# Optimization experiments

Hardware: AMD Instinct MI355X
Metric: run time of the kernel (lower is better)

The kernel has to match this reference:

```python
import jax, jax.numpy as jnp
import numpy as np

D_MODEL, D_INNER, D_STATE, D_CONV, DT_RANK = 2048, 4096, 16, 4, 128
B, T = 2, 1024


def setup_inputs() -> dict:
    key = jax.random.key(0)
    ks = jax.random.split(key, 8)
    dt_init_std = DT_RANK ** -0.5
    # dt bias init per the torch code: inv softplus of dt in [dt_min, dt_max]
    dt = jnp.exp(jax.random.uniform(ks[6], (D_INNER,)) * (np.log(0.1) - np.log(0.001)) + np.log(0.001))
    dt = jnp.clip(dt, 1e-4, None)
    dt_proj_b = dt + jnp.log(-jnp.expm1(-dt))
    A_log = jnp.log(jnp.tile(jnp.arange(1, D_STATE + 1, dtype=jnp.float32)[None, :], (D_INNER, 1)))
    return {
        "x": jax.random.normal(ks[0], (B, T, D_MODEL), jnp.float32),
        "h": jnp.zeros((B, D_INNER, D_STATE), jnp.float32),
        "conv_cache": jnp.zeros((B, D_INNER, D_CONV - 1), jnp.float32),
        "in_proj_w": jax.random.normal(ks[1], (2 * D_INNER, D_MODEL), jnp.float32) * 0.02,
        "conv_w": jax.random.normal(ks[2], (D_INNER, D_CONV), jnp.float32) * (1.0 / np.sqrt(D_CONV)),
        "conv_b": jnp.zeros((D_INNER,), jnp.float32),
        "x_proj_w": jax.random.normal(ks[3], (DT_RANK + 2 * D_STATE, D_INNER), jnp.float32) * 0.02,
        "dt_proj_w": jax.random.uniform(ks[4], (D_INNER, DT_RANK), jnp.float32, -dt_init_std, dt_init_std),
        "dt_proj_b": dt_proj_b,
        "A_log": A_log,
        "D_param": jnp.ones((D_INNER,), jnp.float32),
        "out_proj_w": jax.random.normal(ks[5], (D_MODEL, D_INNER), jnp.float32) * 0.02,
    }


def _forward(x, h, conv_cache, in_proj_w, conv_w, conv_b, x_proj_w,
             dt_proj_w, dt_proj_b, A_log, D_param, out_proj_w):
    Tlen = x.shape[1]
    xz = x @ in_proj_w.T                                  # (B,T,2*d_inner)
    xi, z = jnp.split(xz, 2, axis=-1)
    # causal depthwise conv with cache: concat history then valid conv
    xc = jnp.concatenate([jnp.swapaxes(conv_cache, 1, 2), xi], axis=1)  # (B,T+3,d_inner)
    new_conv_cache = jnp.swapaxes(xc[:, -(D_CONV - 1):, :], 1, 2)       # (B,d_inner,3)
    xconv = sum(xc[:, k:k + Tlen, :] * conv_w[:, k] for k in range(D_CONV)) + conv_b
    xs = jax.nn.silu(xconv)                               # (B,T,d_inner)
    # SSM params per step
    dbc = xs @ x_proj_w.T                                 # (B,T,dt_rank+2n)
    delta, Bm, Cm = jnp.split(dbc, [DT_RANK, DT_RANK + D_STATE], axis=-1)
    delta = jax.nn.softplus(delta @ dt_proj_w.T + dt_proj_b)  # (B,T,d_inner)
    A = -jnp.exp(A_log)                                   # (d_inner,n)
    dA = jnp.exp(jnp.einsum('btd,dn->btdn', delta, A))    # (B,T,d,n)
    dBx = jnp.einsum('btd,btn,btd->btdn', delta, Bm, xs)  # (B,T,d,n)

    def step(hc, inp):
        dA_t, dBx_t, C_t = inp
        hc = dA_t * hc + dBx_t                            # (B,d,n)
        return hc, jnp.einsum('bdn,bn->bd', hc, C_t)

    h_last, ys = jax.lax.scan(
        step, h,
        (jnp.moveaxis(dA, 1, 0), jnp.moveaxis(dBx, 1, 0), jnp.moveaxis(Cm, 1, 0)))
    y = jnp.moveaxis(ys, 0, 1) + D_param * xs             # (B,T,d_inner)
    out = (y * jax.nn.silu(z)) @ out_proj_w.T             # (B,T,d_model)
    return out, h_last, new_conv_cache


def reference(x, h, conv_cache, in_proj_w, conv_w, conv_b, x_proj_w,
              dt_proj_w, dt_proj_b, A_log, D_param, out_proj_w):
    return _forward(x, h, conv_cache, in_proj_w, conv_w, conv_b, x_proj_w,
                    dt_proj_w, dt_proj_b, A_log, D_param, out_proj_w)
```

## Files before the change

kernel.cpp:

```cpp
#include <hip/hip_runtime.h>
#include <hip/hip_bf16.h>
#include <math.h>

#define D_MODEL 2048
#define D_INNER 4096
#define D_STATE 16
#define D_CONV  4
#define DT_RANK 128
#define NB      2
#define TT      1024
#define M_TOT   (NB * TT)
#define NC      16
#define CL      64
#define TC      16

typedef __bf16 bf16x8_t __attribute__((ext_vector_type(8)));
typedef float  f32x4_t  __attribute__((ext_vector_type(4)));

__global__ __launch_bounds__(256) void fused_cast(
    const float* __restrict__ x,  const float* __restrict__ wi,
    const float* __restrict__ wo, const float* __restrict__ wx,
    const float* __restrict__ wdt,
    __bf16* __restrict__ x16,  __bf16* __restrict__ wi16,
    __bf16* __restrict__ wo16, __bf16* __restrict__ wx16,
    __bf16* __restrict__ wdt16, __bf16* __restrict__ dbc16)
{
    const size_t g = (size_t)blockIdx.x * 256 + threadIdx.x;
    const float* src; __bf16* dst; size_t off;
    if      (g < 524288)  { src = x;   dst = x16;   off = g; }
    else if (g < 2621440) { src = wi;  dst = wi16;  off = g - 524288; }
    else if (g < 3670016) { src = wo;  dst = wo16;  off = g - 2621440; }
    else if (g < 3801088) { off = g - 3670016; dst = wx16;
                            src = (g < 3751936) ? wx : nullptr; }
    else if (g < 3866624) { src = wdt; dst = wdt16; off = g - 3801088; }
    else                  { src = nullptr; dst = dbc16; off = g - 3866624; }

    bf16x8_t v;
    if (src) {
        const float4 f0 = ((const float4*)src)[2 * off];
        const float4 f1 = ((const float4*)src)[2 * off + 1];
        v[0] = (__bf16)f0.x; v[1] = (__bf16)f0.y; v[2] = (__bf16)f0.z; v[3] = (__bf16)f0.w;
        v[4] = (__bf16)f1.x; v[5] = (__bf16)f1.y; v[6] = (__bf16)f1.z; v[7] = (__bf16)f1.w;
    } else {
        v = (bf16x8_t)(__bf16)0.f;
    }
    ((bf16x8_t*)dst)[off] = v;
}

template <int EPI, int KSTEP, typename OutT>
__global__ __launch_bounds__(256) void gemm_bf16_nt(
    const __bf16* __restrict__ A, int lda,
    const __bf16* __restrict__ W, int ldw,
    OutT* __restrict__ C, int ldc,
    int Kloop, int Nmax, const float* __restrict__ bias)
{
    __shared__ __bf16 As[128 * KSTEP];
    __shared__ __bf16 Bs[128 * KSTEP];

    const int tid  = threadIdx.x;
    const int wave = tid >> 6;
    const int lane = tid & 63;
    const int m0 = blockIdx.y * 128;
    const int n0 = blockIdx.x * 128;
    const int mw = (wave >> 1) * 64;
    const int nw = (wave & 1) * 64;
    const int koff = blockIdx.z * Kloop;

    f32x4_t acc[4][4] = {};

    const int g0 = wave * 2;
    const int rA = g0 * 16 + (lane >> 2);
    const int kk = (lane & 3) * 8;

    const __bf16* gA0 = A + (size_t)(m0 + rA) * lda + kk + koff;
    const __bf16* gA1 = gA0 + (size_t)16 * lda;
    const __bf16* gB0 = W + (size_t)(n0 + rA) * ldw + kk + koff;
    const __bf16* gB1 = gB0 + (size_t)16 * ldw;

    __bf16* lA0 = &As[(size_t)g0 * 512];
    __bf16* lA1 = &As[(size_t)(g0 + 1) * 512];
    __bf16* lB0 = &Bs[(size_t)g0 * 512];
    __bf16* lB1 = &Bs[(size_t)(g0 + 1) * 512];

    const int fr = lane & 15;
    const int fk = (lane >> 4) * 8;

    for (int k0 = 0; k0 < Kloop; k0 += KSTEP) {
#pragma unroll
        for (int p = 0; p < KSTEP / 32; p++) {
            const int kp = k0 + p * 32;
            const int lp = p * 4096;
            __builtin_amdgcn_global_load_lds(
                (const __attribute__((address_space(1))) void*)(gA0 + kp),
                (__attribute__((address_space(3))) void*)(lA0 + lp), 16, 0, 0);
            __builtin_amdgcn_global_load_lds(
                (const __attribute__((address_space(1))) void*)(gA1 + kp),
                (__attribute__((address_space(3))) void*)(lA1 + lp), 16, 0, 0);
            __builtin_amdgcn_global_load_lds(
                (const __attribute__((address_space(1))) void*)(gB0 + kp),
                (__attribute__((address_space(3))) void*)(lB0 + lp), 16, 0, 0);
            __builtin_amdgcn_global_load_lds(
                (const __attribute__((address_space(1))) void*)(gB1 + kp),
                (__attribute__((address_space(3))) void*)(lB1 + lp), 16, 0, 0);
        }
        __syncthreads();

#pragma unroll
        for (int p = 0; p < KSTEP / 32; p++) {
            const int lp = p * 4096;
            bf16x8_t av[4], bv[4];
#pragma unroll
            for (int mt = 0; mt < 4; mt++)
                av[mt] = *(const bf16x8_t*)&As[lp + (mw + mt * 16 + fr) * 32 + fk];
#pragma unroll
            for (int nt = 0; nt < 4; nt++)
                bv[nt] = *(const bf16x8_t*)&Bs[lp + (nw + nt * 16 + fr) * 32 + fk];

#pragma unroll
            for (int mt = 0; mt < 4; mt++)
#pragma unroll
                for (int nt = 0; nt < 4; nt++)
                    acc[mt][nt] = __builtin_amdgcn_mfma_f32_16x16x32_bf16(
                        av[mt], bv[nt], acc[mt][nt], 0, 0, 0);
        }
        __syncthreads();
    }

    const int cn = n0 + nw + (lane & 15);
    const int rb = m0 + mw + (lane >> 4) * 4;
#pragma unroll
    for (int mt = 0; mt < 4; mt++)
#pragma unroll
        for (int nt = 0; nt < 4; nt++) {
            const int n = cn + nt * 16;
            if (n >= Nmax) continue;
#pragma unroll
            for (int r = 0; r < 4; r++) {
                float v = acc[mt][nt][r];
                OutT* p = &C[(size_t)(rb + mt * 16 + r) * ldc + n];
                if (EPI == 1) {
                    v += bias[n];
                    v = (v > 20.f) ? v : log1pf(__expf(v));
                    *p = (OutT)v;
                } else if (EPI == 2) {
                    atomicAdd((float*)p, v);
                } else {
                    *p = (OutT)v;
                }
            }
        }
}

__global__ __launch_bounds__(256) void gemm_dt(
    const float* __restrict__ A,
    const __bf16* __restrict__ W,
    float* __restrict__ C,
    const float* __restrict__ bias)
{
    __shared__ __bf16 As[128 * 32];
    __shared__ __bf16 Bs[128 * 32];

    const int tid  = threadIdx.x;
    const int wave = tid >> 6;
    const int lane = tid & 63;
    const int m0 = blockIdx.y * 128;
    const int n0 = blockIdx.x * 128;
    const int mw = (wave >> 1) * 64;
    const int nw = (wave & 1) * 64;

    f32x4_t acc[4][4] = {};

    const int g0 = wave * 2;
    const int rA = g0 * 16 + (lane >> 2);
    const int kk = (lane & 3) * 8;

    const float*  gA0 = A + (size_t)(m0 + rA) * 160 + kk;
    const float*  gA1 = gA0 + (size_t)16 * 160;
    const __bf16* gB0 = W + (size_t)(n0 + rA) * 128 + kk;
    const __bf16* gB1 = gB0 + (size_t)16 * 128;

    __bf16* lA0 = &As[(size_t)g0 * 512];
    __bf16* lA1 = &As[(size_t)(g0 + 1) * 512];
    __bf16* lB0 = &Bs[(size_t)g0 * 512];
    __bf16* lB1 = &Bs[(size_t)(g0 + 1) * 512];

    const int fr = lane & 15;
    const int fk = (lane >> 4) * 8;

    for (int k0 = 0; k0 < 128; k0 += 32) {
        const float4 a0 = *(const float4*)(gA0 + k0);
        const float4 a1 = *(const float4*)(gA0 + k0 + 4);
        const float4 a2 = *(const float4*)(gA1 + k0);
        const float4 a3 = *(const float4*)(gA1 + k0 + 4);
        bf16x8_t va, vb;
        va[0] = (__bf16)a0.x; va[1] = (__bf16)a0.y; va[2] = (__bf16)a0.z; va[3] = (__bf16)a0.w;
        va[4] = (__bf16)a1.x; va[5] = (__bf16)a1.y; va[6] = (__bf16)a1.z; va[7] = (__bf16)a1.w;
        vb[0] = (__bf16)a2.x; vb[1] = (__bf16)a2.y; vb[2] = (__bf16)a2.z; vb[3] = (__bf16)a2.w;
        vb[4] = (__bf16)a3.x; vb[5] = (__bf16)a3.y; vb[6] = (__bf16)a3.z; vb[7] = (__bf16)a3.w;
        ((bf16x8_t*)lA0)[lane] = va;
        ((bf16x8_t*)lA1)[lane] = vb;
        __builtin_amdgcn_global_load_lds(
            (const __attribute__((address_space(1))) void*)(gB0 + k0),
            (__attribute__((address_space(3))) void*)lB0, 16, 0, 0);
        __builtin_amdgcn_global_load_lds(
            (const __attribute__((address_space(1))) void*)(gB1 + k0),
            (__attribute__((address_space(3))) void*)lB1, 16, 0, 0);
        __syncthreads();

        bf16x8_t av[4], bv[4];
#pragma unroll
        for (int mt = 0; mt < 4; mt++)
            av[mt] = *(const bf16x8_t*)&As[(mw + mt * 16 + fr) * 32 + fk];
#pragma unroll
        for (int nt = 0; nt < 4; nt++)
            bv[nt] = *(const bf16x8_t*)&Bs[(nw + nt * 16 + fr) * 32 + fk];

#pragma unroll
        for (int mt = 0; mt < 4; mt++)
#pragma unroll
            for (int nt = 0; nt < 4; nt++)
                acc[mt][nt] = __builtin_amdgcn_mfma_f32_16x16x32_bf16(
                    av[mt], bv[nt], acc[mt][nt], 0, 0, 0);
        __syncthreads();
    }

    const int cn = n0 + nw + (lane & 15);
    const int rb = m0 + mw + (lane >> 4) * 4;
#pragma unroll
    for (int mt = 0; mt < 4; mt++)
#pragma unroll
        for (int nt = 0; nt < 4; nt++) {
            const int n = cn + nt * 16;
            const float bs = bias[n];
#pragma unroll
            for (int r = 0; r < 4; r++) {
                float v = acc[mt][nt][r] + bs;
                v = (v > 20.f) ? v : log1pf(__expf(v));
                C[(size_t)(rb + mt * 16 + r) * 4096 + n] = v;
            }
        }
}

__global__ __launch_bounds__(256) void conv_silu(
    const __bf16* __restrict__ xz16,
    const float* __restrict__ conv_cache,
    const float* __restrict__ conv_w,
    const float* __restrict__ conv_b,
    __bf16* __restrict__ xs16,
    float* __restrict__ cc_out)
{
    const int b  = blockIdx.z;
    const int d  = blockIdx.y * 256 + threadIdx.x;
    const int t0 = blockIdx.x * TC;

    const float4 w  = *(const float4*)&conv_w[d * 4];
    const float bias = conv_b[d];

    float v[TC + 3];
    if (t0 == 0) {
        v[0] = conv_cache[(b * D_INNER + d) * 3 + 0];
        v[1] = conv_cache[(b * D_INNER + d) * 3 + 1];
        v[2] = conv_cache[(b * D_INNER + d) * 3 + 2];
    } else {
        v[0] = (float)xz16[(size_t)(b * TT + t0 - 3) * 8192 + d];
        v[1] = (float)xz16[(size_t)(b * TT + t0 - 2) * 8192 + d];
        v[2] = (float)xz16[(size_t)(b * TT + t0 - 1) * 8192 + d];
    }
#pragma unroll
    for (int k = 0; k < TC; k++)
        v[k + 3] = (float)xz16[(size_t)(b * TT + t0 + k) * 8192 + d];

#pragma unroll
    for (int k = 0; k < TC; k++) {
        float c = v[k] * w.x + v[k + 1] * w.y + v[k + 2] * w.z + v[k + 3] * w.w + bias;
        float s = c / (1.f + __expf(-c));
        xs16[(size_t)(b * TT + t0 + k) * 4096 + d] = (__bf16)s;
    }

    if (t0 + TC == TT) {
        cc_out[(b * D_INNER + d) * 3 + 0] = v[TC];
        cc_out[(b * D_INNER + d) * 3 + 1] = v[TC + 1];
        cc_out[(b * D_INNER + d) * 3 + 2] = v[TC + 2];
    }
}

__global__ __launch_bounds__(256) void scan_phase_a(
    const float* __restrict__ delta_p,
    const float* __restrict__ dbc,
    const __bf16* __restrict__ xs16,
    const float* __restrict__ A_log,
    float* __restrict__ P,
    float* __restrict__ S)
{
    const int idx = blockIdx.x * 256 + threadIdx.x;
    const int sub = idx & 3;
    const int d   = (idx >> 2) & 4095;
    const int c   = (idx >> 14) & (NC - 1);
    const int b   = idx >> 18;

    const float4 Af = *(const float4*)&A_log[d * 16 + sub * 4];
    const float Ad0 = -__expf(Af.x), Ad1 = -__expf(Af.y);
    const float Ad2 = -__expf(Af.z), Ad3 = -__expf(Af.w);

    const int t0 = c * CL;
    const float*  pdelta = delta_p + (size_t)(b * TT + t0) * 4096 + d;
    const __bf16* px     = xs16 + (size_t)(b * TT + t0) * 4096 + d;
    const float*  pB     = dbc + ((size_t)b * TT + t0) * 160 + 128 + sub * 4;

    float h0 = 0.f, h1 = 0.f, h2 = 0.f, h3 = 0.f, sd = 0.f;
    for (int t = 0; t < CL; t++) {
        const float delta = pdelta[(size_t)t * 4096];
        const float xv    = (float)px[(size_t)t * 4096];
        const float4 Bv   = *(const float4*)&pB[(size_t)t * 160];
        const float dx = delta * xv;
        h0 = __expf(delta * Ad0) * h0 + dx * Bv.x;
        h1 = __expf(delta * Ad1) * h1 + dx * Bv.y;
        h2 = __expf(delta * Ad2) * h2 + dx * Bv.z;
        h3 = __expf(delta * Ad3) * h3 + dx * Bv.w;
        sd += delta;
    }
    const size_t o = ((size_t)(b * NC + c) * 4096 + d) * 16 + sub * 4;
    *(float4*)&P[o] = make_float4(__expf(Ad0 * sd), __expf(Ad1 * sd),
                                  __expf(Ad2 * sd), __expf(Ad3 * sd));
    *(float4*)&S[o] = make_float4(h0, h1, h2, h3);
}

__global__ __launch_bounds__(256) void scan_phase_c(
    const float* __restrict__ delta_p,
    const __bf16* __restrict__ xz16,
    const float* __restrict__ dbc,
    const __bf16* __restrict__ xs16,
    const float* __restrict__ P,
    const float* __restrict__ S,
    const float* __restrict__ h_in,
    const float* __restrict__ A_log,
    const float* __restrict__ D_param,
    __bf16* __restrict__ ys16,
    float* __restrict__ h_out)
{
    const int idx = blockIdx.x * 256 + threadIdx.x;
    const int sub = idx & 3;
    const int d   = (idx >> 2) & 4095;
    const int c   = (idx >> 14) & (NC - 1);
    const int b   = idx >> 18;

    const float4 Af = *(const float4*)&A_log[d * 16 + sub * 4];
    const float Ad0 = -__expf(Af.x), Ad1 = -__expf(Af.y);
    const float Ad2 = -__expf(Af.z), Ad3 = -__expf(Af.w);
    const float Dp = D_param[d];

    float4 hf = *(const float4*)&h_in[((size_t)b * 4096 + d) * 16 + sub * 4];
    float h0 = hf.x, h1 = hf.y, h2 = hf.z, h3 = hf.w;
    for (int cc = 0; cc < c; cc++) {
        const size_t o2 = ((size_t)(b * NC + cc) * 4096 + d) * 16 + sub * 4;
        const float4 p = *(const float4*)&P[o2];
        const float4 s = *(const float4*)&S[o2];
        h0 = p.x * h0 + s.x;
        h1 = p.y * h1 + s.y;
        h2 = p.z * h2 + s.z;
        h3 = p.w * h3 + s.w;
    }

    const int t0 = c * CL;
    const float*  pdelta = delta_p + (size_t)(b * TT + t0) * 4096 + d;
    const __bf16* pz     = xz16 + (size_t)(b * TT + t0) * 8192 + 4096 + d;
    const __bf16* px     = xs16 + (size_t)(b * TT + t0) * 4096 + d;
    const float*  pB     = dbc + ((size_t)b * TT + t0) * 160 + 128 + sub * 4;
    const float*  pC     = pB + 16;
    __bf16* py = ys16 + (size_t)(b * TT + t0) * 4096 + d;

    for (int t = 0; t < CL; t++) {
        const float delta = pdelta[(size_t)t * 4096];
        const float xv    = (float)px[(size_t)t * 4096];
        const float4 Bv   = *(const float4*)&pB[(size_t)t * 160];
        const float4 Cv   = *(const float4*)&pC[(size_t)t * 160];
        const float dx = delta * xv;

        h0 = __expf(delta * Ad0) * h0 + dx * Bv.x;
        h1 = __expf(delta * Ad1) * h1 + dx * Bv.y;
        h2 = __expf(delta * Ad2) * h2 + dx * Bv.z;
        h3 = __expf(delta * Ad3) * h3 + dx * Bv.w;

        float y = h0 * Cv.x + h1 * Cv.y + h2 * Cv.z + h3 * Cv.w;
        y += __shfl_xor(y, 1);
        y += __shfl_xor(y, 2);

        if (sub == 0) {
            const float zv = (float)pz[(size_t)t * 8192];
            y += Dp * xv;
            const float g = zv / (1.f + __expf(-zv));
            py[(size_t)t * 4096] = (__bf16)(y * g);
        }
    }

    if (c == NC - 1) {
        *(float4*)&h_out[((size_t)b * 4096 + d) * 16 + sub * 4] =
            make_float4(h0, h1, h2, h3);
    }
}

extern "C" void kernel_launch(void* const* d_in, const int* in_sizes, int n_in,
                              void* d_out, int out_size, void* d_ws, size_t ws_size,
                              hipStream_t stream)
{
    const float* x          = (const float*)d_in[0];
    const float* h_in       = (const float*)d_in[1];
    const float* conv_cache = (const float*)d_in[2];
    const float* in_proj_w  = (const float*)d_in[3];
    const float* conv_w     = (const float*)d_in[4];
    const float* conv_b     = (const float*)d_in[5];
    const float* x_proj_w   = (const float*)d_in[6];
    const float* dt_proj_w  = (const float*)d_in[7];
    const float* dt_proj_b  = (const float*)d_in[8];
    const float* A_log      = (const float*)d_in[9];
    const float* D_param    = (const float*)d_in[10];
    const float* out_proj_w = (const float*)d_in[11];

    float* out    = (float*)d_out;
    float* h_out  = (float*)d_out + (size_t)NB * TT * D_MODEL;
    float* cc_out = h_out + (size_t)NB * D_INNER * D_STATE;

    float* Pbuf = out;
    float* Sbuf = out + 2097152;

    char* ws = (char*)d_ws;
    __bf16* xz16  = (__bf16*)(ws);
    __bf16* x16   = (__bf16*)(ws + 33554432);
    __bf16* wi16  = (__bf16*)(ws + 41943040);
    float*  delta = (float*)(ws + 41943040);
    __bf16* wo16  = (__bf16*)(ws + 75497472);
    __bf16* xs16  = (__bf16*)(ws + 92274688);
    float*  dbc   = (float*)(ws + 109051904);
    __bf16* ys16  = (__bf16*)(ws + 110362624);
    __bf16* wx16  = (__bf16*)(ws + 127139840);
    __bf16* wdt16 = (__bf16*)(ws + 129236992);

    dim3 blk(256);

    fused_cast<<<dim3(15424), blk, 0, stream>>>(
        x, in_proj_w, out_proj_w, x_proj_w, dt_proj_w,
        x16, wi16, wo16, wx16, wdt16, (__bf16*)dbc);

    gemm_bf16_nt<0, 64, __bf16><<<dim3(64, 16, 1), blk, 0, stream>>>(
        x16, 2048, wi16, 2048, xz16, 8192, 2048, 8192, nullptr);

    conv_silu<<<dim3(TT / TC, D_INNER / 256, NB), blk, 0, stream>>>(
        xz16, conv_cache, conv_w, conv_b, xs16, cc_out);

    gemm_bf16_nt<2, 32, float><<<dim3(2, 16, 8), blk, 0, stream>>>(
        xs16, 4096, wx16, 4096, dbc, 160, 512, 160, nullptr);

    gemm_dt<<<dim3(32, 16), blk, 0, stream>>>(dbc, wdt16, delta, dt_proj_b);

    scan_phase_a<<<dim3(NB * D_INNER * NC * 4 / 256), blk, 0, stream>>>(
        delta, dbc, xs16, A_log, Pbuf, Sbuf);
    scan_phase_c<<<dim3(NB * D_INNER * NC * 4 / 256), blk, 0, stream>>>(
        delta, xz16, dbc, xs16, Pbuf, Sbuf, h_in, A_log, D_param, ys16, h_out);

    hipMemsetAsync(out, 0, (size_t)M_TOT * D_MODEL * 4, stream);
    gemm_bf16_nt<2, 64, float><<<dim3(16, 16, 4), blk, 0, stream>>>(
        ys16, 4096, wo16, 4096, out, 2048, 1024, 2048, nullptr);
}
```

Measured before the change: 504.8 us.

## Store delta in bf16, zero output in cast kernel, rebalance split-K

The dt-projection GEMM now writes softplus(delta) as bf16, which halves the delta traffic read by both scan phases. The P/S chunk buffers move from the output buffer into workspace. This lets the output be zeroed inside the fused cast kernel, replacing the separate memset. Split-K factors change: x_proj uses 16 splits instead of 8 and out_proj uses 2 instead of 4, which reduces atomic traffic on the output. The scan loops also get unroll hints. The cost is that delta loses precision, which can shift accuracy through exp(delta*A) in the scan.

```diff
diff --git a/kernel.cpp b/kernel.cpp
--- a/kernel.cpp
+++ b/kernel.cpp
@@ -23,7 +23,8 @@
     const float* __restrict__ wdt,
     __bf16* __restrict__ x16,  __bf16* __restrict__ wi16,
     __bf16* __restrict__ wo16, __bf16* __restrict__ wx16,
-    __bf16* __restrict__ wdt16, __bf16* __restrict__ dbc16)
+    __bf16* __restrict__ wdt16, __bf16* __restrict__ dbc16,
+    __bf16* __restrict__ out16)
 {
     const size_t g = (size_t)blockIdx.x * 256 + threadIdx.x;
     const float* src; __bf16* dst; size_t off;
@@ -33,7 +34,8 @@
     else if (g < 3801088) { off = g - 3670016; dst = wx16;
                             src = (g < 3751936) ? wx : nullptr; }
     else if (g < 3866624) { src = wdt; dst = wdt16; off = g - 3801088; }
-    else                  { src = nullptr; dst = dbc16; off = g - 3866624; }
+    else if (g < 3948544) { src = nullptr; dst = dbc16; off = g - 3866624; }
+    else                  { src = nullptr; dst = out16; off = g - 3948544; }
 
     bf16x8_t v;
     if (src) {
@@ -154,7 +156,7 @@
 __global__ __launch_bounds__(256) void gemm_dt(
     const float* __restrict__ A,
     const __bf16* __restrict__ W,
-    float* __restrict__ C,
+    __bf16* __restrict__ C,
     const float* __restrict__ bias)
 {
     __shared__ __bf16 As[128 * 32];
@@ -236,7 +238,7 @@
             for (int r = 0; r < 4; r++) {
                 float v = acc[mt][nt][r] + bs;
                 v = (v > 20.f) ? v : log1pf(__expf(v));
-                C[(size_t)(rb + mt * 16 + r) * 4096 + n] = v;
+                C[(size_t)(rb + mt * 16 + r) * 4096 + n] = (__bf16)v;
             }
         }
 }
@@ -285,7 +287,7 @@
 }
 
 __global__ __launch_bounds__(256) void scan_phase_a(
-    const float* __restrict__ delta_p,
+    const __bf16* __restrict__ delta16,
     const float* __restrict__ dbc,
     const __bf16* __restrict__ xs16,
     const float* __restrict__ A_log,
@@ -303,13 +305,14 @@
     const float Ad2 = -__expf(Af.z), Ad3 = -__expf(Af.w);
 
     const int t0 = c * CL;
-    const float*  pdelta = delta_p + (size_t)(b * TT + t0) * 4096 + d;
+    const __bf16* pdelta = delta16 + (size_t)(b * TT + t0) * 4096 + d;
     const __bf16* px     = xs16 + (size_t)(b * TT + t0) * 4096 + d;
     const float*  pB     = dbc + ((size_t)b * TT + t0) * 160 + 128 + sub * 4;
 
     float h0 = 0.f, h1 = 0.f, h2 = 0.f, h3 = 0.f, sd = 0.f;
+#pragma unroll 4
     for (int t = 0; t < CL; t++) {
-        const float delta = pdelta[(size_t)t * 4096];
+        const float delta = (float)pdelta[(size_t)t * 4096];
         const float xv    = (float)px[(size_t)t * 4096];
         const float4 Bv   = *(const float4*)&pB[(size_t)t * 160];
         const float dx = delta * xv;
@@ -326,7 +329,7 @@
 }
 
 __global__ __launch_bounds__(256) void scan_phase_c(
-    const float* __restrict__ delta_p,
+    const __bf16* __restrict__ delta16,
     const __bf16* __restrict__ xz16,
     const float* __restrict__ dbc,
     const __bf16* __restrict__ xs16,
@@ -362,15 +365,16 @@
     }
 
     const int t0 = c * CL;
-    const float*  pdelta = delta_p + (size_t)(b * TT + t0) * 4096 + d;
+    const __bf16* pdelta = delta16 + (size_t)(b * TT + t0) * 4096 + d;
     const __bf16* pz     = xz16 + (size_t)(b * TT + t0) * 8192 + 4096 + d;
     const __bf16* px     = xs16 + (size_t)(b * TT + t0) * 4096 + d;
     const float*  pB     = dbc + ((size_t)b * TT + t0) * 160 + 128 + sub * 4;
     const float*  pC     = pB + 16;
     __bf16* py = ys16 + (size_t)(b * TT + t0) * 4096 + d;
 
+#pragma unroll 4
     for (int t = 0; t < CL; t++) {
-        const float delta = pdelta[(size_t)t * 4096];
+        const float delta = (float)pdelta[(size_t)t * 4096];
         const float xv    = (float)px[(size_t)t * 4096];
         const float4 Bv   = *(const float4*)&pB[(size_t)t * 160];
         const float4 Cv   = *(const float4*)&pC[(size_t)t * 160];
@@ -420,26 +424,25 @@
     float* h_out  = (float*)d_out + (size_t)NB * TT * D_MODEL;
     float* cc_out = h_out + (size_t)NB * D_INNER * D_STATE;
 
-    float* Pbuf = out;
-    float* Sbuf = out + 2097152;
-
     char* ws = (char*)d_ws;
-    __bf16* xz16  = (__bf16*)(ws);
-    __bf16* x16   = (__bf16*)(ws + 33554432);
-    __bf16* wi16  = (__bf16*)(ws + 41943040);
-    float*  delta = (float*)(ws + 41943040);
-    __bf16* wo16  = (__bf16*)(ws + 75497472);
-    __bf16* xs16  = (__bf16*)(ws + 92274688);
-    float*  dbc   = (float*)(ws + 109051904);
-    __bf16* ys16  = (__bf16*)(ws + 110362624);
-    __bf16* wx16  = (__bf16*)(ws + 127139840);
-    __bf16* wdt16 = (__bf16*)(ws + 129236992);
+    __bf16* xz16    = (__bf16*)(ws);
+    __bf16* x16     = (__bf16*)(ws + 33554432);
+    float*  Pbuf    = (float*)(ws + 33554432);
+    __bf16* wi16    = (__bf16*)(ws + 41943040);
+    __bf16* delta16 = (__bf16*)(ws + 41943040);
+    float*  Sbuf    = (float*)(ws + 58720256);
+    __bf16* wo16    = (__bf16*)(ws + 75497472);
+    __bf16* xs16    = (__bf16*)(ws + 92274688);
+    float*  dbc     = (float*)(ws + 109051904);
+    __bf16* ys16    = (__bf16*)(ws + 110362624);
+    __bf16* wx16    = (__bf16*)(ws + 127139840);
+    __bf16* wdt16   = (__bf16*)(ws + 129236992);
 
     dim3 blk(256);
 
-    fused_cast<<<dim3(15424), blk, 0, stream>>>(
+    fused_cast<<<dim3(19520), blk, 0, stream>>>(
         x, in_proj_w, out_proj_w, x_proj_w, dt_proj_w,
-        x16, wi16, wo16, wx16, wdt16, (__bf16*)dbc);
+        x16, wi16, wo16, wx16, wdt16, (__bf16*)dbc, (__bf16*)out);
 
     gemm_bf16_nt<0, 64, __bf16><<<dim3(64, 16, 1), blk, 0, stream>>>(
         x16, 2048, wi16, 2048, xz16, 8192, 2048, 8192, nullptr);
@@ -447,17 +450,16 @@
     conv_silu<<<dim3(TT / TC, D_INNER / 256, NB), blk, 0, stream>>>(
         xz16, conv_cache, conv_w, conv_b, xs16, cc_out);
 
-    gemm_bf16_nt<2, 32, float><<<dim3(2, 16, 8), blk, 0, stream>>>(
-        xs16, 4096, wx16, 4096, dbc, 160, 512, 160, nullptr);
-
-    gemm_dt<<<dim3(32, 16), blk, 0, stream>>>(dbc, wdt16, delta, dt_proj_b);
+    gemm_bf16_nt<2, 32, float><<<dim3(2, 16, 16), blk, 0, stream>>>(
+        xs16, 4096, wx16, 4096, dbc, 160, 256, 160, nullptr);
+
+    gemm_dt<<<dim3(32, 16), blk, 0, stream>>>(dbc, wdt16, delta16, dt_proj_b);
 
     scan_phase_a<<<dim3(NB * D_INNER * NC * 4 / 256), blk, 0, stream>>>(
-        delta, dbc, xs16, A_log, Pbuf, Sbuf);
+        delta16, dbc, xs16, A_log, Pbuf, Sbuf);
     scan_phase_c<<<dim3(NB * D_INNER * NC * 4 / 256), blk, 0, stream>>>(
-        delta, xz16, dbc, xs16, Pbuf, Sbuf, h_in, A_log, D_param, ys16, h_out);
-
-    hipMemsetAsync(out, 0, (size_t)M_TOT * D_MODEL * 4, stream);
-    gemm_bf16_nt<2, 64, float><<<dim3(16, 16, 4), blk, 0, stream>>>(
-        ys16, 4096, wo16, 4096, out, 2048, 1024, 2048, nullptr);
-}
+        delta16, xz16, dbc, xs16, Pbuf, Sbuf, h_in, A_log, D_param, ys16, h_out);
+
+    gemm_bf16_nt<2, 64, float><<<dim3(16, 16, 2), blk, 0, stream>>>(
+        ys16, 4096, wo16, 4096, out, 2048, 2048, 2048, nullptr);
+}
```

Result: faster. 489.3 us (-3.1%).
